# Kernel optimization log

Measured on AMD Instinct MI355X. Metric: run time of the kernel, lower is better.

The kernel has to match this reference:

```python
import jax, jax.numpy as jnp
import numpy as np


def setup_inputs() -> dict:
    key = jax.random.key(0)
    ks = jax.random.split(key, 7)
    B, C, W, H = 4, 128, 64, 64
    Cq = C // 8
    x = jax.random.normal(ks[0], (B, C, W, H), jnp.float32)
    wq = jax.random.normal(ks[1], (Cq, C), jnp.float32) * 0.05
    bq = jax.random.normal(ks[2], (Cq,), jnp.float32) * 0.05
    wk = jax.random.normal(ks[3], (Cq, C), jnp.float32) * 0.05
    bk = jax.random.normal(ks[4], (Cq,), jnp.float32) * 0.05
    wv = jax.random.normal(ks[5], (C, C), jnp.float32) * 0.05
    bv = jax.random.normal(ks[6], (C,), jnp.float32) * 0.05
    gamma = jnp.ones((1,), jnp.float32)
    return {"x": x, "wq": wq, "bq": bq, "wk": wk, "bk": bk,
            "wv": wv, "bv": bv, "gamma": gamma}


def reference(x, wq, bq, wk, bk, wv, bv, gamma):
    B, C, W, H = x.shape
    N = W * H
    xf = x.reshape(B, C, N)  # flatten spatial dims (W fastest over H, as torch .view)
    # 1x1 convs == per-position linear maps
    q = jnp.einsum('dc,bcn->bnd', wq, xf) + bq            # [B, N, C//8]
    k = jnp.einsum('dc,bcn->bdn', wk, xf) + bk[:, None]   # [B, C//8, N]
    v = jnp.einsum('dc,bcn->bdn', wv, xf) + bv[:, None]   # [B, C, N]
    energy = jnp.einsum('bnd,bdm->bnm', q, k)             # [B, N, N]
    # block-causal mask: position i may attend only to j < (i//W + 1)*W
    i = jnp.arange(N)
    j = jnp.arange(N)
    masked = j[None, :] >= ((i[:, None] // W) + 1) * W    # True -> -inf
    energy = jnp.where(masked[None, :, :], -jnp.inf, energy)
    attention = jax.nn.softmax(energy, axis=-1)           # [B, N, N]
    # out[b,c,n] = sum_m V[b,c,m] * attn[b,n,m]  (torch bmm(V, attn^T))
    out = jnp.einsum('bcm,bnm->bcn', v, attention).reshape(B, C, W, H)
    out = gamma * out + x
    return (out, attention)
```

## Files before the change

### kernel.cpp

```cpp
#include <hip/hip_runtime.h>
#include <hip/hip_bf16.h>


typedef __attribute__((ext_vector_type(8))) short short8;
typedef __attribute__((ext_vector_type(16))) float float16;
typedef __attribute__((ext_vector_type(4))) float floatx4;

__device__ __forceinline__ ushort f2bf(float f) {
  union { float f; uint u; } v; v.f = f;
  return (ushort)((v.u + 0x7FFFu + ((v.u >> 16) & 1u)) >> 16);
}

__global__ __launch_bounds__(512, 2) void qkv_kernel(
    const float* __restrict__ x,
    const float* __restrict__ wq, const float* __restrict__ bq,
    const float* __restrict__ wk, const float* __restrict__ bk,
    const float* __restrict__ wv, const float* __restrict__ bv,
    ushort* __restrict__ qT, ushort* __restrict__ kT, ushort* __restrict__ vo) {
  __shared__ float xs[128 * 64];
  const int nt = blockIdx.x, b = blockIdx.y;
  const int n0 = nt * 64;
  const float* xb = x + (size_t)b * 524288 + n0;
  for (int idx = threadIdx.x; idx < 8192; idx += 512) {
    int c = idx >> 6, n = idx & 63;
    xs[idx] = xb[(size_t)c * 4096 + n];
  }
  __syncthreads();
  const int n = threadIdx.x & 63;
  const int og = __builtin_amdgcn_readfirstlane((int)(threadIdx.x >> 6));
  float acc[20];
#pragma unroll
  for (int i = 0; i < 20; i++) {
    int o = og + 8 * i;
    acc[i] = (i < 2) ? bq[o] : (i < 4) ? bk[o - 16] : bv[o - 32];
  }
#pragma unroll 4
  for (int c = 0; c < 128; c++) {
    float xr = xs[c * 64 + n];
#pragma unroll
    for (int i = 0; i < 20; i++) {
      int o = og + 8 * i;
      const float* wr = (i < 2) ? (wq + o * 128)
                      : (i < 4) ? (wk + (o - 16) * 128)
                                : (wv + (o - 32) * 128);
      acc[i] += wr[c] * xr;
    }
  }
  const size_t pos = (size_t)b * 4096 + n0 + n;
#pragma unroll
  for (int i = 0; i < 20; i++) {
    int o = og + 8 * i;
    if (i < 2)      qT[pos * 16 + o]      = f2bf(acc[i]);
    else if (i < 4) kT[pos * 16 + o - 16] = f2bf(acc[i]);
    else vo[(size_t)b * 524288 + (size_t)(o - 32) * 4096 + n0 + n] = f2bf(acc[i]);
  }
}

__global__ __launch_bounds__(256, 2) void denom_kernel(
    const ushort* __restrict__ qT, const ushort* __restrict__ kT,
    float* __restrict__ invw) {
  __shared__ float red[32][4];
  const int bx = blockIdx.x;
  const int b = bx & 3;
  const int v_ = bx >> 2;
  const int half = v_ & 1;
  const int u = v_ >> 1;
  const int rb = (u < 32) ? u : 95 - u;
  const int S = rb + 1;
  const int lane = threadIdx.x & 63;
  const int w = __builtin_amdgcn_readfirstlane((int)(threadIdx.x >> 6));
  const int nblk = rb * 64 + half * 32;
  const int l31 = lane & 31;
  const int h = lane >> 5;
  const int hk = h * 8;
  const ushort* qb = qT + (size_t)b * 65536;
  const ushort* kb = kT + (size_t)b * 65536;
  const short8 qa = *(const short8*)(qb + (size_t)(nblk + l31) * 16 + hk);
  float16 zero16;
#pragma unroll
  for (int i = 0; i < 16; i++) zero16[i] = 0.f;

  float sume[16];
#pragma unroll
  for (int i = 0; i < 16; i++) sume[i] = 0.f;
  for (int s = w; s < S; s += 4) {
    const int m0 = s * 64;
#pragma unroll
    for (int mh = 0; mh < 2; mh++) {
      short8 kf = *(const short8*)(kb + (size_t)(m0 + mh * 32 + l31) * 16 + hk);
      float16 e = __builtin_amdgcn_mfma_f32_32x32x16_bf16(qa, kf, zero16, 0, 0, 0);
#pragma unroll
      for (int r = 0; r < 16; r++) sume[r] += __expf(e[r]);
    }
  }
#pragma unroll
  for (int r = 0; r < 16; r++) {
#pragma unroll
    for (int off = 1; off <= 16; off <<= 1)
      sume[r] += __shfl_xor(sume[r], off, 64);
  }
  if (l31 == 0) {
#pragma unroll
    for (int r = 0; r < 16; r++) {
      int row = (r & 3) + 8 * (r >> 2) + 4 * h;
      red[row][w] = sume[r];
    }
  }
  __syncthreads();
  if (w == 0 && l31 == 0) {
#pragma unroll
    for (int r = 0; r < 16; r++) {
      int row = (r & 3) + 8 * (r >> 2) + 4 * h;
      float4 p4 = *(const float4*)&red[row][0];
      invw[(size_t)b * 4096 + nblk + row] = 1.0f / (p4.x + p4.y + p4.z + p4.w);
    }
  }
}

__global__ __launch_bounds__(256, 4) void attn_write_kernel(
    const ushort* __restrict__ qT, const ushort* __restrict__ kT,
    const float* __restrict__ invw, float* __restrict__ attn) {
  const int bx = blockIdx.x;
  const int b = bx & 3;
  const int ch = (bx >> 2) & 1;
  const int v_ = bx >> 3;
  const int half = v_ & 1;
  const int u = v_ >> 1;
  const int rb = (u < 32) ? u : 95 - u;
  const int S = rb + 1;
  const int M = S * 64;
  const int lane = threadIdx.x & 63;
  const int w = __builtin_amdgcn_readfirstlane((int)(threadIdx.x >> 6));
  const int nblk = rb * 64 + half * 32;
  const int l31 = lane & 31;
  const int h = lane >> 5;
  const int hk = h * 8;
  const ushort* qb = qT + (size_t)b * 65536;
  const ushort* kb = kT + (size_t)b * 65536;
  float* ab = attn + (size_t)b * 16777216;

  const short8 qa = *(const short8*)(qb + (size_t)(nblk + l31) * 16 + hk);
  float inv_r[16];
#pragma unroll
  for (int r = 0; r < 16; r++) {
    int row = (r & 3) + 8 * (r >> 2) + 4 * h;
    inv_r[r] = invw[(size_t)b * 4096 + nblk + row];
  }
  float16 zero16;
#pragma unroll
  for (int i = 0; i < 16; i++) zero16[i] = 0.f;

  const int sEnd = (S < ch * 32 + 32) ? S : (ch * 32 + 32);
  for (int s = ch * 32 + w; s < sEnd; s += 4) {
    const int m0 = s * 64;
#pragma unroll
    for (int mh = 0; mh < 2; mh++) {
      short8 kf = *(const short8*)(kb + (size_t)(m0 + mh * 32 + l31) * 16 + hk);
      float16 e = __builtin_amdgcn_mfma_f32_32x32x16_bf16(qa, kf, zero16, 0, 0, 0);
#pragma unroll
      for (int r = 0; r < 16; r++) {
        int row = (r & 3) + 8 * (r >> 2) + 4 * h;
        float p = __expf(e[r]) * inv_r[r];
        __builtin_nontemporal_store(
            p, &ab[(size_t)(nblk + row) * 4096 + m0 + mh * 32 + l31]);
      }
    }
  }

  const int zc0 = (M > ch * 2048) ? M : ch * 2048;
  const int zc1 = (ch + 1) * 2048;
  if (zc0 < zc1) {
    const int Z4 = (zc1 - zc0) >> 2;
    const floatx4 z = {0.f, 0.f, 0.f, 0.f};
#pragma unroll
    for (int r = 0; r < 8; r++) {
      floatx4* dst = (floatx4*)(ab + (size_t)(nblk + w * 8 + r) * 4096 + zc0);
      for (int i4 = lane; i4 < Z4; i4 += 64)
        __builtin_nontemporal_store(z, &dst[i4]);
    }
  }
}

__global__ __launch_bounds__(256, 2) void pv_kernel(
    const ushort* __restrict__ qT, const ushort* __restrict__ kT,
    const ushort* __restrict__ vws, const float* __restrict__ invw,
    const float* __restrict__ x, const float* __restrict__ g,
    float* __restrict__ out) {
  __shared__ __align__(16) ushort Pt[4][32 * 72];
  const int bx = blockIdx.x;
  const int b = bx & 3;
  const int v_ = bx >> 2;
  const int half = v_ & 1;
  const int u = v_ >> 1;
  const int rb = (u < 32) ? u : 95 - u;
  const int S = rb + 1;
  const int lane = threadIdx.x & 63;
  const int w = __builtin_amdgcn_readfirstlane((int)(threadIdx.x >> 6));
  const int nblk = rb * 64 + half * 32;
  const int l31 = lane & 31;
  const int h = lane >> 5;
  const int hk = h * 8;
  const ushort* qb = qT + (size_t)b * 65536;
  const ushort* kb = kT + (size_t)b * 65536;
  const ushort* vp = vws + (size_t)b * 524288;

  const short8 qa = *(const short8*)(qb + (size_t)(nblk + l31) * 16 + hk);
  float inv_r[16];
#pragma unroll
  for (int r = 0; r < 16; r++) {
    int row = (r & 3) + 8 * (r >> 2) + 4 * h;
    inv_r[r] = invw[(size_t)b * 4096 + nblk + row];
  }
  float16 zero16;
#pragma unroll
  for (int i = 0; i < 16; i++) zero16[i] = 0.f;

  float16 acc = zero16;
  for (int s0 = 0; s0 < S; s0 += 4) {
    const int sl = (S - s0 < 4) ? (S - s0) : 4;
    if (w < sl) {
      const int m0 = (s0 + w) * 64;
      ushort* Pb = &Pt[w][0];
#pragma unroll
      for (int mh = 0; mh < 2; mh++) {
        short8 kf = *(const short8*)(kb + (size_t)(m0 + mh * 32 + l31) * 16 + hk);
        float16 e = __builtin_amdgcn_mfma_f32_32x32x16_bf16(qa, kf, zero16, 0, 0, 0);
#pragma unroll
        for (int r = 0; r < 16; r++) {
          int row = (r & 3) + 8 * (r >> 2) + 4 * h;
          float p = __expf(e[r]) * inv_r[r];
          Pb[row * 72 + mh * 32 + l31] = f2bf(p);
        }
      }
    }
    __syncthreads();
    for (int ss = 0; ss < sl; ss++) {
      const int m0 = (s0 + ss) * 64;
      const ushort* vrow = vp + (size_t)(w * 32 + l31) * 4096 + m0 + hk;
      const ushort* Pr = &Pt[ss][l31 * 72 + hk];
#pragma unroll
      for (int kk = 0; kk < 4; kk++) {
        short8 a  = *(const short8*)(vrow + kk * 16);
        short8 bf = *(const short8*)(Pr + kk * 16);
        acc = __builtin_amdgcn_mfma_f32_32x32x16_bf16(a, bf, acc, 0, 0, 0);
      }
    }
    __syncthreads();
  }

  const float gamma = g[0];
#pragma unroll
  for (int reg = 0; reg < 16; reg++) {
    int row = (reg & 3) + 8 * (reg >> 2) + 4 * h;
    int c = w * 32 + row;
    int n = nblk + l31;
    size_t off = (size_t)b * 524288 + (size_t)c * 4096 + n;
    out[off] = gamma * acc[reg] + x[off];
  }
}

extern "C" void kernel_launch(void* const* d_in, const int* in_sizes, int n_in,
                              void* d_out, int out_size, void* d_ws, size_t ws_size,
                              hipStream_t stream) {
  const float* x  = (const float*)d_in[0];
  const float* wq = (const float*)d_in[1];
  const float* bq = (const float*)d_in[2];
  const float* wk = (const float*)d_in[3];
  const float* bk = (const float*)d_in[4];
  const float* wv = (const float*)d_in[5];
  const float* bv = (const float*)d_in[6];
  const float* gm = (const float*)d_in[7];
  float* out  = (float*)d_out;
  float* attn = out + 2097152;
  ushort* qTw = (ushort*)d_ws;
  ushort* kTw = qTw + 262144;
  ushort* vws = qTw + 524288;
  float* invw = (float*)(qTw + 2621440);

  qkv_kernel<<<dim3(64, 4), 512, 0, stream>>>(x, wq, bq, wk, bk, wv, bv, qTw, kTw, vws);
  denom_kernel<<<dim3(512), 256, 0, stream>>>(qTw, kTw, invw);
  attn_write_kernel<<<dim3(1024), 256, 0, stream>>>(qTw, kTw, invw, attn);
  pv_kernel<<<dim3(512), 256, 0, stream>>>(qTw, kTw, vws, invw, x, gm, out);
}
```

Baseline: 400.5 us.

## Fuse softmax denominator and attention write into one kernel

Merges the denominator pass and the attention-matrix write kernel into a single kernel. Row-sum reciprocals now come straight from shared memory and are reused in the same block for writing normalized probabilities. This removes one launch and the global round trip for the inverse sums. In exchange the grid shrinks from 1024 to 512 blocks at 2 waves/SIMD occupancy instead of 4, and stores change from nontemporal to regular, which could lower write bandwidth on the 256MB attention output.

Result: no change. 400.5 us (-0.0%).

```diff
diff --git a/kernel.cpp b/kernel.cpp
--- a/kernel.cpp
+++ b/kernel.cpp
@@ -56,9 +56,9 @@
   }
 }
 
-__global__ __launch_bounds__(256, 2) void denom_kernel(
+__global__ __launch_bounds__(256, 2) void smwrite_kernel(
     const ushort* __restrict__ qT, const ushort* __restrict__ kT,
-    float* __restrict__ invw) {
+    float* __restrict__ invw, float* __restrict__ attn) {
   __shared__ float red[32][4];
   const int bx = blockIdx.x;
   const int b = bx & 3;
@@ -75,6 +75,8 @@
   const int hk = h * 8;
   const ushort* qb = qT + (size_t)b * 65536;
   const ushort* kb = kT + (size_t)b * 65536;
+  float* ab = attn + (size_t)b * 16777216;
+
   const short8 qa = *(const short8*)(qb + (size_t)(nblk + l31) * 16 + hk);
   float16 zero16;
 #pragma unroll
@@ -107,51 +109,22 @@
     }
   }
   __syncthreads();
+  float inv_r[16];
+#pragma unroll
+  for (int r = 0; r < 16; r++) {
+    int row = (r & 3) + 8 * (r >> 2) + 4 * h;
+    float4 p4 = *(const float4*)&red[row][0];
+    inv_r[r] = 1.0f / (p4.x + p4.y + p4.z + p4.w);
+  }
   if (w == 0 && l31 == 0) {
 #pragma unroll
     for (int r = 0; r < 16; r++) {
       int row = (r & 3) + 8 * (r >> 2) + 4 * h;
-      float4 p4 = *(const float4*)&red[row][0];
-      invw[(size_t)b * 4096 + nblk + row] = 1.0f / (p4.x + p4.y + p4.z + p4.w);
-    }
-  }
-}
-
-__global__ __launch_bounds__(256, 4) void attn_write_kernel(
-    const ushort* __restrict__ qT, const ushort* __restrict__ kT,
-    const float* __restrict__ invw, float* __restrict__ attn) {
-  const int bx = blockIdx.x;
-  const int b = bx & 3;
-  const int ch = (bx >> 2) & 1;
-  const int v_ = bx >> 3;
-  const int half = v_ & 1;
-  const int u = v_ >> 1;
-  const int rb = (u < 32) ? u : 95 - u;
-  const int S = rb + 1;
-  const int M = S * 64;
-  const int lane = threadIdx.x & 63;
-  const int w = __builtin_amdgcn_readfirstlane((int)(threadIdx.x >> 6));
-  const int nblk = rb * 64 + half * 32;
-  const int l31 = lane & 31;
-  const int h = lane >> 5;
-  const int hk = h * 8;
-  const ushort* qb = qT + (size_t)b * 65536;
-  const ushort* kb = kT + (size_t)b * 65536;
-  float* ab = attn + (size_t)b * 16777216;
-
-  const short8 qa = *(const short8*)(qb + (size_t)(nblk + l31) * 16 + hk);
-  float inv_r[16];
-#pragma unroll
-  for (int r = 0; r < 16; r++) {
-    int row = (r & 3) + 8 * (r >> 2) + 4 * h;
-    inv_r[r] = invw[(size_t)b * 4096 + nblk + row];
-  }
-  float16 zero16;
-#pragma unroll
-  for (int i = 0; i < 16; i++) zero16[i] = 0.f;
-
-  const int sEnd = (S < ch * 32 + 32) ? S : (ch * 32 + 32);
-  for (int s = ch * 32 + w; s < sEnd; s += 4) {
+      invw[(size_t)b * 4096 + nblk + row] = inv_r[r];
+    }
+  }
+
+  for (int s = w; s < S; s += 4) {
     const int m0 = s * 64;
 #pragma unroll
     for (int mh = 0; mh < 2; mh++) {
@@ -161,23 +134,18 @@
       for (int r = 0; r < 16; r++) {
         int row = (r & 3) + 8 * (r >> 2) + 4 * h;
         float p = __expf(e[r]) * inv_r[r];
-        __builtin_nontemporal_store(
-            p, &ab[(size_t)(nblk + row) * 4096 + m0 + mh * 32 + l31]);
+        ab[(size_t)(nblk + row) * 4096 + m0 + mh * 32 + l31] = p;
       }
     }
   }
 
-  const int zc0 = (M > ch * 2048) ? M : ch * 2048;
-  const int zc1 = (ch + 1) * 2048;
-  if (zc0 < zc1) {
-    const int Z4 = (zc1 - zc0) >> 2;
-    const floatx4 z = {0.f, 0.f, 0.f, 0.f};
-#pragma unroll
-    for (int r = 0; r < 8; r++) {
-      floatx4* dst = (floatx4*)(ab + (size_t)(nblk + w * 8 + r) * 4096 + zc0);
-      for (int i4 = lane; i4 < Z4; i4 += 64)
-        __builtin_nontemporal_store(z, &dst[i4]);
-    }
+  const int M = S * 64;
+  const int Z4 = (4096 - M) >> 2;
+  const floatx4 z = {0.f, 0.f, 0.f, 0.f};
+#pragma unroll
+  for (int r = 0; r < 8; r++) {
+    floatx4* dst = (floatx4*)(ab + (size_t)(nblk + w * 8 + r) * 4096 + M);
+    for (int i4 = lane; i4 < Z4; i4 += 64) dst[i4] = z;
   }
 }
 
@@ -278,7 +246,6 @@
   float* invw = (float*)(qTw + 2621440);
 
   qkv_kernel<<<dim3(64, 4), 512, 0, stream>>>(x, wq, bq, wk, bk, wv, bv, qTw, kTw, vws);
-  denom_kernel<<<dim3(512), 256, 0, stream>>>(qTw, kTw, invw);
-  attn_write_kernel<<<dim3(1024), 256, 0, stream>>>(qTw, kTw, invw, attn);
+  smwrite_kernel<<<dim3(512), 256, 0, stream>>>(qTw, kTw, invw, attn);
   pv_kernel<<<dim3(512), 256, 0, stream>>>(qTw, kTw, vws, invw, x, gm, out);
 }
```
